# Performance work log

Hardware: AMD Instinct MI355X
Metric: run time of the kernel (lower is better)

Reference implementation:

```python
import jax, jax.numpy as jnp
import numpy as np

B, S, D = 2, 2048, 2048
H, KVH = 16, 4
HD = D // H            # 128
N_REP = H // KVH       # 4


def apply_rope(x, cos, sin):
    # x: (b, s, h, hd); cos/sin: (1, s, 1, hd//2)
    b, s, h, hd = x.shape
    xr = x.reshape(b, s, h, hd // 2, 2)
    p1, p2 = xr[..., 0], xr[..., 1]
    # Original concatenates rotated halves (does NOT re-interleave).
    return jnp.concatenate([p1 * cos - p2 * sin, p2 * cos + p1 * sin], axis=-1)


def setup_inputs() -> dict:
    key = jax.random.key(0)
    ks = jax.random.split(key, 8)
    hidden_states = jax.random.normal(ks[0], (B, S, D), dtype=jnp.float32)
    # additive causal mask (0 on/below diagonal, -1e9 above)
    mask = jnp.where(jnp.tril(jnp.ones((S, S), dtype=bool)), 0.0, -1e9).astype(jnp.float32)
    attention_mask = mask[None, None, :, :]
    cos = jax.random.normal(ks[1], (1, S, 1, HD // 2), dtype=jnp.float32)
    sin = jax.random.normal(ks[2], (1, S, 1, HD // 2), dtype=jnp.float32)
    sc = 1.0 / np.sqrt(D)
    Wq = jax.random.normal(ks[3], (D, H * HD), dtype=jnp.float32) * sc
    Wk = jax.random.normal(ks[4], (D, KVH * HD), dtype=jnp.float32) * sc
    Wv = jax.random.normal(ks[5], (D, KVH * HD), dtype=jnp.float32) * sc
    Wo = jax.random.normal(ks[6], (H * HD, D), dtype=jnp.float32) * sc
    return {"hidden_states": hidden_states, "attention_mask": attention_mask,
            "cos": cos, "sin": sin, "Wq": Wq, "Wk": Wk, "Wv": Wv, "Wo": Wo}


def reference(hidden_states, attention_mask, cos, sin, Wq, Wk, Wv, Wo):
    b, s, _ = hidden_states.shape
    q = (hidden_states @ Wq).reshape(b, s, H, HD)
    k = (hidden_states @ Wk).reshape(b, s, KVH, HD)
    v = (hidden_states @ Wv).reshape(b, s, KVH, HD)
    q = apply_rope(q, cos, sin)
    k = apply_rope(k, cos, sin)
    # GQA: repeat kv heads contiguously (matches expand+reshape)
    k = jnp.repeat(k, N_REP, axis=2)
    v = jnp.repeat(v, N_REP, axis=2)
    # (b, h, s, hd)
    q = q.transpose(0, 2, 1, 3)
    k = k.transpose(0, 2, 1, 3)
    v = v.transpose(0, 2, 1, 3)
    scores = jnp.einsum('bhqd,bhkd->bhqk', q, k) / np.sqrt(HD).astype(np.float32)
    scores = scores + attention_mask
    attn = jax.nn.softmax(scores.astype(jnp.float32), axis=-1)
    out = jnp.einsum('bhqk,bhkd->bhqd', attn, v)
    out = out.transpose(0, 2, 1, 3).reshape(b, s, H * HD)
    return out @ Wo
```

## Files before the change

kernel.cpp:

```cpp
#include <hip/hip_runtime.h>
#include <cstddef>
#include <cstdint>

#define S_LEN 2048
#define DMODEL 2048
#define NH 16
#define NKV 4
#define HD 128
#define BATCH 2
#define MROWS (BATCH * S_LEN)
#define KVD (NKV * HD)
#define QKVSTR 3072
#define NQT (S_LEN / 64)

typedef __attribute__((ext_vector_type(8))) short bf16x8;
typedef __attribute__((ext_vector_type(4))) float floatx4;
typedef __attribute__((ext_vector_type(8))) _Float16 half8;
typedef __attribute__((ext_vector_type(4))) _Float16 half4;
typedef __attribute__((ext_vector_type(2))) _Float16 half2v;

#define QSCALE 0.1275310255f

__device__ inline short f2bf(float f) {
  union { float f; unsigned u; } v; v.f = f;
  unsigned r = v.u + 0x7FFFu + ((v.u >> 16) & 1u);
  return (short)(r >> 16);
}

__device__ inline half2v pack2h(float lo, float hi) {
  union { decltype(__builtin_amdgcn_cvt_pkrtz(0.f, 0.f)) raw; half2v h; } u;
  u.raw = __builtin_amdgcn_cvt_pkrtz(lo, hi);
  return u.h;
}

__device__ __forceinline__ void glds16(const void* g, void* l) {
  __builtin_amdgcn_global_load_lds(
      reinterpret_cast<const int __attribute__((address_space(1)))*>(
          reinterpret_cast<uintptr_t>(g)),
      reinterpret_cast<int __attribute__((address_space(3)))*>(
          reinterpret_cast<uintptr_t>(l)),
      16, 0, 0);
}

__global__ __launch_bounds__(256) void cast_bf16(
    const float* __restrict__ x, short* __restrict__ y)
{
  const size_t i = ((size_t)blockIdx.x * 256 + threadIdx.x) * 8;
  const float4 a = *(const float4*)(x + i);
  const float4 b = *(const float4*)(x + i + 4);
  bf16x8 o;
  o[0] = f2bf(a.x); o[1] = f2bf(a.y); o[2] = f2bf(a.z); o[3] = f2bf(a.w);
  o[4] = f2bf(b.x); o[5] = f2bf(b.y); o[6] = f2bf(b.z); o[7] = f2bf(b.w);
  *(bf16x8*)(y + i) = o;
}

__global__ __launch_bounds__(256) void tcast(
    const float* __restrict__ W, short* __restrict__ Wt, int N)
{
  __shared__ float Ts[64][65];
  const int n0 = blockIdx.x * 64, k0 = blockIdx.y * 64;
  const int tid = threadIdx.x;
#pragma unroll
  for (int it = 0; it < 4; ++it) {
    const int r = it * 16 + (tid >> 4);
    *(float4*)&Ts[r][(tid & 15) * 4] =
        *(const float4*)&W[(size_t)(k0 + r) * N + n0 + (tid & 15) * 4];
  }
  __syncthreads();
  const int n = tid >> 2, kg = (tid & 3) * 16;
  bf16x8 o0, o1;
#pragma unroll
  for (int e = 0; e < 8; ++e) o0[e] = f2bf(Ts[kg + e][n]);
#pragma unroll
  for (int e = 0; e < 8; ++e) o1[e] = f2bf(Ts[kg + 8 + e][n]);
  short* dst = Wt + (size_t)(n0 + n) * DMODEL + k0 + kg;
  *(bf16x8*)dst = o0;
  *(bf16x8*)(dst + 8) = o1;
}

template <bool OUTF16>
__global__ __launch_bounds__(256) void gemm_glds(
    const short* __restrict__ A, const short* __restrict__ Bt,
    void* __restrict__ Cv, int M, int N, int K)
{
  __shared__ short As[128 * 64];
  __shared__ short Bs[128 * 64];

  const int tid = threadIdx.x;
  const int wave = tid >> 6, lane = tid & 63;
  const int l16 = lane & 15, quad = lane >> 4;
  const int wm = (wave & 1) * 64, wn = (wave >> 1) * 64;
  const int m0 = blockIdx.y * 128, n0 = blockIdx.x * 128;

  const short* Ab = A + (size_t)(m0 + wave * 32 + (lane >> 3)) * K + ((lane & 7) << 3);
  const short* Bb = Bt + (size_t)(n0 + wave * 32 + (lane >> 3)) * K + ((lane & 7) << 3);
  short* Asw = As + wave * 32 * 64;
  short* Bsw = Bs + wave * 32 * 64;

  floatx4 acc[4][4];
#pragma unroll
  for (int i = 0; i < 4; ++i)
#pragma unroll
    for (int j = 0; j < 4; ++j)
#pragma unroll
      for (int r = 0; r < 4; ++r) acc[i][j][r] = 0.f;

  for (int k0 = 0; k0 < K; k0 += 64) {
    __syncthreads();
#pragma unroll
    for (int u = 0; u < 4; ++u) {
      glds16(Ab + (size_t)(u * 8) * K + k0, Asw + u * 8 * 64);
      glds16(Bb + (size_t)(u * 8) * K + k0, Bsw + u * 8 * 64);
    }
    __syncthreads();
#pragma unroll
    for (int c = 0; c < 2; ++c) {
      bf16x8 af[4], bf[4];
#pragma unroll
      for (int i = 0; i < 4; ++i)
        af[i] = *(const bf16x8*)&As[(wm + i * 16 + l16) * 64 + c * 32 + quad * 8];
#pragma unroll
      for (int j = 0; j < 4; ++j)
        bf[j] = *(const bf16x8*)&Bs[(wn + j * 16 + l16) * 64 + c * 32 + quad * 8];
#pragma unroll
      for (int i = 0; i < 4; ++i)
#pragma unroll
        for (int j = 0; j < 4; ++j)
          acc[i][j] = __builtin_amdgcn_mfma_f32_16x16x32_bf16(af[i], bf[j], acc[i][j], 0, 0, 0);
    }
  }

#pragma unroll
  for (int i = 0; i < 4; ++i)
#pragma unroll
    for (int r = 0; r < 4; ++r) {
      const int row = m0 + wm + i * 16 + (quad << 2) + r;
      if (OUTF16) {
        _Float16* cr = (_Float16*)Cv + (size_t)row * N + n0 + wn + l16;
#pragma unroll
        for (int j = 0; j < 4; ++j) cr[j * 16] = (_Float16)acc[i][j][r];
      } else {
        float* cr = (float*)Cv + (size_t)row * N + n0 + wn + l16;
#pragma unroll
        for (int j = 0; j < 4; ++j) cr[j * 16] = acc[i][j][r];
      }
    }
}

__global__ __launch_bounds__(256) void rope_k(
    _Float16* __restrict__ kh, const float* __restrict__ cosp,
    const float* __restrict__ sinp)
{
  const int row = blockIdx.x * 4 + (threadIdx.x >> 6);
  const int sl = row & (S_LEN - 1);
  const int t = threadIdx.x & 63;
  const int h = t >> 4, g = t & 15;
  _Float16* base = kh + (size_t)row * QKVSTR + h * HD;
  const half8 x = *(const half8*)(base + 8 * g);
  const float4 c4 = *(const float4*)&cosp[sl * 64 + 4 * g];
  const float4 s4 = *(const float4*)&sinp[sl * 64 + 4 * g];
  const float p1[4] = {(float)x[0], (float)x[2], (float)x[4], (float)x[6]};
  const float p2[4] = {(float)x[1], (float)x[3], (float)x[5], (float)x[7]};
  const float cc[4] = {c4.x, c4.y, c4.z, c4.w};
  const float ss[4] = {s4.x, s4.y, s4.z, s4.w};
  __syncthreads();
  half4 o1, o2;
#pragma unroll
  for (int u = 0; u < 4; ++u) {
    o1[u] = (_Float16)(p1[u] * cc[u] - p2[u] * ss[u]);
    o2[u] = (_Float16)(p2[u] * cc[u] + p1[u] * ss[u]);
  }
  *(half4*)(base + 4 * g) = o1;
  *(half4*)(base + 64 + 4 * g) = o2;
}

__global__ __launch_bounds__(256) void vtprep(
    const _Float16* __restrict__ v, _Float16* __restrict__ Vt)
{
  __shared__ _Float16 Ts[64][72];
  const int s0 = blockIdx.x * 64, c0 = blockIdx.y * 64;
  const int tid = threadIdx.x;
#pragma unroll
  for (int it = 0; it < 4; ++it) {
    const int r = it * 16 + (tid >> 4);
    *(half4*)&Ts[r][(tid & 15) * 4] =
        *(const half4*)&v[(size_t)(s0 + r) * QKVSTR + c0 + (tid & 15) * 4];
  }
  __syncthreads();
  const int dr = tid >> 2, sg = tid & 3;
  const int d = c0 + dr;
  const int kvh = d >> 7, dd = d & 127;
  const int bb = s0 >> 11, sl = s0 & (S_LEN - 1);
  half8 t0, t1;
#pragma unroll
  for (int kk = 0; kk < 8; ++kk) t0[kk] = Ts[sg * 16 + kk][dr];
#pragma unroll
  for (int kk = 0; kk < 8; ++kk) t1[kk] = Ts[sg * 16 + 8 + kk][dr];
  _Float16* dst = Vt + ((size_t)(bb * NKV + kvh) * HD + dd) * S_LEN + sl + sg * 16;
  *(half8*)dst = t0;
  *(half8*)(dst + 8) = t1;
}

__global__ __launch_bounds__(256, 3) void attn_mfma(
    const _Float16* __restrict__ Qh, const _Float16* __restrict__ Kr,
    const _Float16* __restrict__ Vt, const float* __restrict__ cosp,
    const float* __restrict__ sinp, short* __restrict__ aout)
{
  __shared__ _Float16 Ks[64][136];
  __shared__ _Float16 Vs[128][72];
  __shared__ _Float16 Ps[4][16][72];

  const int tid = threadIdx.x;
  const int wave = tid >> 6, lane = tid & 63;
  const int l16 = lane & 15, quad = lane >> 4;
  const int pair = blockIdx.x;
  const int h = blockIdx.y, b = blockIdx.z;
  const int kvh = h >> 2;

  const int skr = tid >> 2;
  const int skc = (tid & 3) * 32;
  const _Float16* kgp = Kr + (size_t)(b * S_LEN + skr) * QKVSTR + kvh * HD + skc;
  const int svr = tid >> 1;
  const int svc = (tid & 1) * 32;
  const _Float16* vgp = Vt + ((size_t)(b * NKV + kvh) * HD + svr) * S_LEN + svc;

  for (int pass = 0; pass < 2; ++pass) {
    const int qt = pass ? (NQT - 1 - pair) : pair;
    const int q0 = qt * 64 + wave * 16;
    const int srow = q0 + l16;

    half8 qf[4];
    {
      const _Float16* qraw = Qh + (size_t)(b * S_LEN + srow) * QKVSTR + h * HD;
#pragma unroll
      for (int cc = 0; cc < 2; ++cc) {
        const half8 r0 = *(const half8*)(qraw + cc * 64 + quad * 16);
        const half8 r1 = *(const half8*)(qraw + cc * 64 + quad * 16 + 8);
        const float4 c0 = *(const float4*)&cosp[srow % S_LEN * 64 + cc * 32 + quad * 8];
        const float4 c1 = *(const float4*)&cosp[srow % S_LEN * 64 + cc * 32 + quad * 8 + 4];
        const float4 s0 = *(const float4*)&sinp[srow % S_LEN * 64 + cc * 32 + quad * 8];
        const float4 s1 = *(const float4*)&sinp[srow % S_LEN * 64 + cc * 32 + quad * 8 + 4];
        const float cA[8] = {c0.x, c0.y, c0.z, c0.w, c1.x, c1.y, c1.z, c1.w};
        const float sA[8] = {s0.x, s0.y, s0.z, s0.w, s1.x, s1.y, s1.z, s1.w};
#pragma unroll
        for (int j = 0; j < 8; ++j) {
          const float p1 = (float)((j < 4) ? r0[2 * j] : r1[2 * (j - 4)]);
          const float p2 = (float)((j < 4) ? r0[2 * j + 1] : r1[2 * (j - 4) + 1]);
          qf[cc][j]     = (_Float16)((p1 * cA[j] - p2 * sA[j]) * QSCALE);
          qf[cc + 2][j] = (_Float16)((p2 * cA[j] + p1 * sA[j]) * QSCALE);
        }
      }
    }

    floatx4 o[8];
#pragma unroll
    for (int d = 0; d < 8; ++d) o[d] = (floatx4){0.f, 0.f, 0.f, 0.f};
    float m_run[4] = {-3e38f, -3e38f, -3e38f, -3e38f};
    float l_run[4] = {0.f, 0.f, 0.f, 0.f};

    for (int kt = 0; kt <= qt; ++kt) {
      const int k0 = kt * 64;
      __syncthreads();
      {
        const _Float16* g = kgp + (size_t)k0 * QKVSTR;
        _Float16* dst = &Ks[skr][skc];
#pragma unroll
        for (int u = 0; u < 4; ++u)
          *(half8*)(dst + u * 8) = *(const half8*)(g + u * 8);
      }
      {
        const _Float16* g = vgp + k0;
        _Float16* dst = &Vs[svr][svc];
#pragma unroll
        for (int u = 0; u < 4; ++u)
          *(half8*)(dst + u * 8) = *(const half8*)(g + u * 8);
      }
      __syncthreads();

      floatx4 s[4];
#pragma unroll
      for (int i = 0; i < 4; ++i) {
        s[i] = (floatx4){0.f, 0.f, 0.f, 0.f};
#pragma unroll
        for (int c = 0; c < 4; ++c) {
          const half8 kf = *(const half8*)&Ks[i * 16 + l16][quad * 8 + c * 32];
          s[i] = __builtin_amdgcn_mfma_f32_16x16x32_f16(qf[c], kf, s[i], 0, 0, 0);
        }
      }

      if (kt == qt) {
#pragma unroll
        for (int i = 0; i < 4; ++i) {
          const int kpos = k0 + i * 16 + l16;
#pragma unroll
          for (int r = 0; r < 4; ++r)
            if (kpos > q0 + quad * 4 + r) s[i][r] = -3.0e38f;
        }
      }

      float p[4][4];
#pragma unroll
      for (int r = 0; r < 4; ++r) {
        float rm = fmaxf(fmaxf(s[0][r], s[1][r]), fmaxf(s[2][r], s[3][r]));
        rm = fmaxf(rm, __shfl_xor(rm, 1));
        rm = fmaxf(rm, __shfl_xor(rm, 2));
        rm = fmaxf(rm, __shfl_xor(rm, 4));
        rm = fmaxf(rm, __shfl_xor(rm, 8));
        const float mnew = fmaxf(m_run[r], rm);
        const float alpha = exp2f(m_run[r] - mnew);
        m_run[r] = mnew;
        float rs = 0.f;
#pragma unroll
        for (int i = 0; i < 4; ++i) { p[i][r] = exp2f(s[i][r] - mnew); rs += p[i][r]; }
        rs += __shfl_xor(rs, 1);
        rs += __shfl_xor(rs, 2);
        rs += __shfl_xor(rs, 4);
        rs += __shfl_xor(rs, 8);
        l_run[r] = l_run[r] * alpha + rs;
#pragma unroll
        for (int d = 0; d < 8; ++d) o[d][r] *= alpha;
      }

      const int odd = l16 & 1;
      const int cbase = l16 & 14;
#pragma unroll
      for (int i = 0; i < 4; ++i) {
#pragma unroll
        for (int rr = 0; rr < 2; ++rr) {
          const float send = odd ? p[i][rr] : p[i][2 + rr];
          const float recv = __shfl_xor(send, 1);
          const float lo = odd ? recv : p[i][rr];
          const float hi = odd ? p[i][2 + rr] : recv;
          *(half2v*)&Ps[wave][quad * 4 + 2 * odd + rr][i * 16 + cbase] = pack2h(lo, hi);
        }
      }
      const half8 pf0 = *(const half8*)&Ps[wave][l16][quad * 8];
      const half8 pf1 = *(const half8*)&Ps[wave][l16][32 + quad * 8];

#pragma unroll
      for (int d = 0; d < 8; ++d) {
        const half8 vf0 = *(const half8*)&Vs[d * 16 + l16][quad * 8];
        const half8 vf1 = *(const half8*)&Vs[d * 16 + l16][32 + quad * 8];
        o[d] = __builtin_amdgcn_mfma_f32_16x16x32_f16(pf0, vf0, o[d], 0, 0, 0);
        o[d] = __builtin_amdgcn_mfma_f32_16x16x32_f16(pf1, vf1, o[d], 0, 0, 0);
      }
    }

    float inv[4];
#pragma unroll
    for (int r = 0; r < 4; ++r) inv[r] = 1.0f / l_run[r];
#pragma unroll
    for (int d = 0; d < 8; ++d)
#pragma unroll
      for (int r = 0; r < 4; ++r)
        aout[(size_t)(b * S_LEN + q0 + quad * 4 + r) * DMODEL + h * HD + d * 16 + l16] =
            f2bf(o[d][r] * inv[r]);
  }
}

extern "C" void kernel_launch(void* const* d_in, const int* in_sizes, int n_in,
                              void* d_out, int out_size, void* d_ws, size_t ws_size,
                              hipStream_t stream) {
  const float* hs   = (const float*)d_in[0];
  const float* cosp = (const float*)d_in[2];
  const float* sinp = (const float*)d_in[3];
  const float* Wq   = (const float*)d_in[4];
  const float* Wk   = (const float*)d_in[5];
  const float* Wv   = (const float*)d_in[6];
  const float* Wo   = (const float*)d_in[7];
  float* out = (float*)d_out;

  char* w = (char*)d_ws;
  short*    hsb = (short*)w;
  short*    Wt  = (short*)(w + 16777216);
  _Float16* qkv = (_Float16*)(w + 29360128);
  _Float16* Vt  = (_Float16*)(w + 54525952);
  short*    ao  = hsb;

  _Float16* qh = qkv;
  _Float16* kh = qkv + 2048;
  _Float16* vh = qkv + 2560;

  dim3 blk(256);
  cast_bf16<<<MROWS * DMODEL / (8 * 256), blk, 0, stream>>>(hs, hsb);
  tcast<<<dim3(DMODEL / 64, DMODEL / 64), blk, 0, stream>>>(Wq, Wt, DMODEL);
  tcast<<<dim3(KVD / 64, DMODEL / 64), blk, 0, stream>>>(Wk, Wt + (size_t)2048 * DMODEL, KVD);
  tcast<<<dim3(KVD / 64, DMODEL / 64), blk, 0, stream>>>(Wv, Wt + (size_t)2560 * DMODEL, KVD);
  gemm_glds<true><<<dim3(QKVSTR / 128, MROWS / 128), blk, 0, stream>>>(hsb, Wt, qkv, MROWS, QKVSTR, DMODEL);
  rope_k<<<MROWS / 4, blk, 0, stream>>>(kh, cosp, sinp);
  vtprep<<<dim3(MROWS / 64, KVD / 64), blk, 0, stream>>>(vh, Vt);
  attn_mfma<<<dim3(NQT / 2, NH, BATCH), blk, 0, stream>>>(qh, kh, Vt, cosp, sinp, ao);
  tcast<<<dim3(DMODEL / 64, DMODEL / 64), blk, 0, stream>>>(Wo, Wt, DMODEL);
  gemm_glds<false><<<dim3(DMODEL / 128, MROWS / 128), blk, 0, stream>>>(ao, Wt, out, MROWS, DMODEL, DMODEL);
}
```

Baseline: 395.6 us.

## Double-buffer K/V tiles with register prefetch in attention kernel

The attention kernel now keeps two LDS buffers for K and V. It issues the global loads for the next tile into registers before computing on the current tile, then stores them into the alternate buffer afterwards, so global latency can overlap MFMA work and one barrier per iteration is removed. MFMA sections are wrapped with s_setprio, and the online-softmax rescale runs only when the row max grows. The extra LDS lowers the occupancy hint from 3 to 2 blocks per CU, and holding the prefetched tile in registers raises register pressure.

```diff
diff --git a/kernel.cpp b/kernel.cpp
--- a/kernel.cpp
+++ b/kernel.cpp
@@ -201,13 +201,13 @@
   *(half8*)(dst + 8) = t1;
 }
 
-__global__ __launch_bounds__(256, 3) void attn_mfma(
+__global__ __launch_bounds__(256, 2) void attn_mfma(
     const _Float16* __restrict__ Qh, const _Float16* __restrict__ Kr,
     const _Float16* __restrict__ Vt, const float* __restrict__ cosp,
     const float* __restrict__ sinp, short* __restrict__ aout)
 {
-  __shared__ _Float16 Ks[64][136];
-  __shared__ _Float16 Vs[128][72];
+  __shared__ _Float16 Ks[2][64][136];
+  __shared__ _Float16 Vs[2][128][72];
   __shared__ _Float16 Ps[4][16][72];
 
   const int tid = threadIdx.x;
@@ -258,35 +258,49 @@
     float m_run[4] = {-3e38f, -3e38f, -3e38f, -3e38f};
     float l_run[4] = {0.f, 0.f, 0.f, 0.f};
 
+    __syncthreads();
+    {
+      _Float16* dst = &Ks[0][skr][skc];
+#pragma unroll
+      for (int u = 0; u < 4; ++u)
+        *(half8*)(dst + u * 8) = *(const half8*)(kgp + u * 8);
+      _Float16* dv = &Vs[0][svr][svc];
+#pragma unroll
+      for (int u = 0; u < 4; ++u)
+        *(half8*)(dv + u * 8) = *(const half8*)(vgp + u * 8);
+    }
+    __syncthreads();
+
+    int cur = 0;
     for (int kt = 0; kt <= qt; ++kt) {
       const int k0 = kt * 64;
-      __syncthreads();
-      {
-        const _Float16* g = kgp + (size_t)k0 * QKVSTR;
-        _Float16* dst = &Ks[skr][skc];
-#pragma unroll
-        for (int u = 0; u < 4; ++u)
-          *(half8*)(dst + u * 8) = *(const half8*)(g + u * 8);
-      }
-      {
-        const _Float16* g = vgp + k0;
-        _Float16* dst = &Vs[svr][svc];
-#pragma unroll
-        for (int u = 0; u < 4; ++u)
-          *(half8*)(dst + u * 8) = *(const half8*)(g + u * 8);
-      }
-      __syncthreads();
+      const bool pre = (kt < qt);
+
+      half8 kreg[4], vreg[4];
+      if (pre) {
+        const _Float16* g = kgp + (size_t)(kt + 1) * 64 * QKVSTR;
+#pragma unroll
+        for (int u = 0; u < 4; ++u) kreg[u] = *(const half8*)(g + u * 8);
+        const _Float16* gv = vgp + (kt + 1) * 64;
+#pragma unroll
+        for (int u = 0; u < 4; ++u) vreg[u] = *(const half8*)(gv + u * 8);
+      }
+
+      const _Float16 (*Kc)[136] = Ks[cur];
+      const _Float16 (*Vc)[72]  = Vs[cur];
 
       floatx4 s[4];
+      __builtin_amdgcn_s_setprio(1);
 #pragma unroll
       for (int i = 0; i < 4; ++i) {
         s[i] = (floatx4){0.f, 0.f, 0.f, 0.f};
 #pragma unroll
         for (int c = 0; c < 4; ++c) {
-          const half8 kf = *(const half8*)&Ks[i * 16 + l16][quad * 8 + c * 32];
+          const half8 kf = *(const half8*)&Kc[i * 16 + l16][quad * 8 + c * 32];
           s[i] = __builtin_amdgcn_mfma_f32_16x16x32_f16(qf[c], kf, s[i], 0, 0, 0);
         }
       }
+      __builtin_amdgcn_s_setprio(0);
 
       if (kt == qt) {
 #pragma unroll
@@ -306,19 +320,21 @@
         rm = fmaxf(rm, __shfl_xor(rm, 2));
         rm = fmaxf(rm, __shfl_xor(rm, 4));
         rm = fmaxf(rm, __shfl_xor(rm, 8));
-        const float mnew = fmaxf(m_run[r], rm);
-        const float alpha = exp2f(m_run[r] - mnew);
-        m_run[r] = mnew;
+        if (rm > m_run[r]) {
+          const float alpha = exp2f(m_run[r] - rm);
+          m_run[r] = rm;
+          l_run[r] *= alpha;
+#pragma unroll
+          for (int d = 0; d < 8; ++d) o[d][r] *= alpha;
+        }
         float rs = 0.f;
 #pragma unroll
-        for (int i = 0; i < 4; ++i) { p[i][r] = exp2f(s[i][r] - mnew); rs += p[i][r]; }
+        for (int i = 0; i < 4; ++i) { p[i][r] = exp2f(s[i][r] - m_run[r]); rs += p[i][r]; }
         rs += __shfl_xor(rs, 1);
         rs += __shfl_xor(rs, 2);
         rs += __shfl_xor(rs, 4);
         rs += __shfl_xor(rs, 8);
-        l_run[r] = l_run[r] * alpha + rs;
-#pragma unroll
-        for (int d = 0; d < 8; ++d) o[d][r] *= alpha;
+        l_run[r] += rs;
       }
 
       const int odd = l16 & 1;
@@ -337,13 +353,26 @@
       const half8 pf0 = *(const half8*)&Ps[wave][l16][quad * 8];
       const half8 pf1 = *(const half8*)&Ps[wave][l16][32 + quad * 8];
 
+      __builtin_amdgcn_s_setprio(1);
 #pragma unroll
       for (int d = 0; d < 8; ++d) {
-        const half8 vf0 = *(const half8*)&Vs[d * 16 + l16][quad * 8];
-        const half8 vf1 = *(const half8*)&Vs[d * 16 + l16][32 + quad * 8];
+        const half8 vf0 = *(const half8*)&Vc[d * 16 + l16][quad * 8];
+        const half8 vf1 = *(const half8*)&Vc[d * 16 + l16][32 + quad * 8];
         o[d] = __builtin_amdgcn_mfma_f32_16x16x32_f16(pf0, vf0, o[d], 0, 0, 0);
         o[d] = __builtin_amdgcn_mfma_f32_16x16x32_f16(pf1, vf1, o[d], 0, 0, 0);
       }
+      __builtin_amdgcn_s_setprio(0);
+
+      if (pre) {
+        _Float16* dst = &Ks[cur ^ 1][skr][skc];
+#pragma unroll
+        for (int u = 0; u < 4; ++u) *(half8*)(dst + u * 8) = kreg[u];
+        _Float16* dv = &Vs[cur ^ 1][svr][svc];
+#pragma unroll
+        for (int u = 0; u < 4; ++u) *(half8*)(dv + u * 8) = vreg[u];
+      }
+      __syncthreads();
+      cur ^= 1;
     }
 
     float inv[4];
```

Measured after the change: 396.1 us. Within noise of the previous version (+0.1%).

## Launch one attention block per query tile, heaviest first, with MFMA priority hints

Applied to the files above, without the earlier changes.

Replaces the paired light/heavy query-tile scheme with one block per query tile. Heads are mapped to the fastest grid dimension, and blocks are ordered from the longest causal range to the shortest, which doubles the block count and lets the scheduler balance load dynamically. It also raises wave priority around the MFMA sections with s_setprio and skips the rescale of the output accumulator when the running max does not grow. The cost is that each block now loads Q and applies rope once per tile, and the new branch inside the softmax can cause divergence.

```diff
diff --git a/kernel.cpp b/kernel.cpp
--- a/kernel.cpp
+++ b/kernel.cpp
@@ -213,8 +213,8 @@
   const int tid = threadIdx.x;
   const int wave = tid >> 6, lane = tid & 63;
   const int l16 = lane & 15, quad = lane >> 4;
-  const int pair = blockIdx.x;
-  const int h = blockIdx.y, b = blockIdx.z;
+  const int h = blockIdx.x, b = blockIdx.z;
+  const int qt = (NQT - 1) - blockIdx.y;
   const int kvh = h >> 2;
 
   const int skr = tid >> 2;
@@ -224,138 +224,142 @@
   const int svc = (tid & 1) * 32;
   const _Float16* vgp = Vt + ((size_t)(b * NKV + kvh) * HD + svr) * S_LEN + svc;
 
-  for (int pass = 0; pass < 2; ++pass) {
-    const int qt = pass ? (NQT - 1 - pair) : pair;
-    const int q0 = qt * 64 + wave * 16;
-    const int srow = q0 + l16;
-
-    half8 qf[4];
+  const int q0 = qt * 64 + wave * 16;
+  const int srow = q0 + l16;
+
+  half8 qf[4];
+  {
+    const _Float16* qraw = Qh + (size_t)(b * S_LEN + srow) * QKVSTR + h * HD;
+    const int co = (srow & (S_LEN - 1)) * 64;
+#pragma unroll
+    for (int cc = 0; cc < 2; ++cc) {
+      const half8 r0 = *(const half8*)(qraw + cc * 64 + quad * 16);
+      const half8 r1 = *(const half8*)(qraw + cc * 64 + quad * 16 + 8);
+      const float4 c0 = *(const float4*)&cosp[co + cc * 32 + quad * 8];
+      const float4 c1 = *(const float4*)&cosp[co + cc * 32 + quad * 8 + 4];
+      const float4 s0 = *(const float4*)&sinp[co + cc * 32 + quad * 8];
+      const float4 s1 = *(const float4*)&sinp[co + cc * 32 + quad * 8 + 4];
+      const float cA[8] = {c0.x, c0.y, c0.z, c0.w, c1.x, c1.y, c1.z, c1.w};
+      const float sA[8] = {s0.x, s0.y, s0.z, s0.w, s1.x, s1.y, s1.z, s1.w};
+#pragma unroll
+      for (int j = 0; j < 8; ++j) {
+        const float p1 = (float)((j < 4) ? r0[2 * j] : r1[2 * (j - 4)]);
+        const float p2 = (float)((j < 4) ? r0[2 * j + 1] : r1[2 * (j - 4) + 1]);
+        qf[cc][j]     = (_Float16)((p1 * cA[j] - p2 * sA[j]) * QSCALE);
+        qf[cc + 2][j] = (_Float16)((p2 * cA[j] + p1 * sA[j]) * QSCALE);
+      }
+    }
+  }
+
+  floatx4 o[8];
+#pragma unroll
+  for (int d = 0; d < 8; ++d) o[d] = (floatx4){0.f, 0.f, 0.f, 0.f};
+  float m_run[4] = {-3e38f, -3e38f, -3e38f, -3e38f};
+  float l_run[4] = {0.f, 0.f, 0.f, 0.f};
+
+  for (int kt = 0; kt <= qt; ++kt) {
+    const int k0 = kt * 64;
+    __syncthreads();
     {
-      const _Float16* qraw = Qh + (size_t)(b * S_LEN + srow) * QKVSTR + h * HD;
-#pragma unroll
-      for (int cc = 0; cc < 2; ++cc) {
-        const half8 r0 = *(const half8*)(qraw + cc * 64 + quad * 16);
-        const half8 r1 = *(const half8*)(qraw + cc * 64 + quad * 16 + 8);
-        const float4 c0 = *(const float4*)&cosp[srow % S_LEN * 64 + cc * 32 + quad * 8];
-        const float4 c1 = *(const float4*)&cosp[srow % S_LEN * 64 + cc * 32 + quad * 8 + 4];
-        const float4 s0 = *(const float4*)&sinp[srow % S_LEN * 64 + cc * 32 + quad * 8];
-        const float4 s1 = *(const float4*)&sinp[srow % S_LEN * 64 + cc * 32 + quad * 8 + 4];
-        const float cA[8] = {c0.x, c0.y, c0.z, c0.w, c1.x, c1.y, c1.z, c1.w};
-        const float sA[8] = {s0.x, s0.y, s0.z, s0.w, s1.x, s1.y, s1.z, s1.w};
-#pragma unroll
-        for (int j = 0; j < 8; ++j) {
-          const float p1 = (float)((j < 4) ? r0[2 * j] : r1[2 * (j - 4)]);
-          const float p2 = (float)((j < 4) ? r0[2 * j + 1] : r1[2 * (j - 4) + 1]);
-          qf[cc][j]     = (_Float16)((p1 * cA[j] - p2 * sA[j]) * QSCALE);
-          qf[cc + 2][j] = (_Float16)((p2 * cA[j] + p1 * sA[j]) * QSCALE);
-        }
-      }
-    }
-
-    floatx4 o[8];
-#pragma unroll
-    for (int d = 0; d < 8; ++d) o[d] = (floatx4){0.f, 0.f, 0.f, 0.f};
-    float m_run[4] = {-3e38f, -3e38f, -3e38f, -3e38f};
-    float l_run[4] = {0.f, 0.f, 0.f, 0.f};
-
-    for (int kt = 0; kt <= qt; ++kt) {
-      const int k0 = kt * 64;
-      __syncthreads();
-      {
-        const _Float16* g = kgp + (size_t)k0 * QKVSTR;
-        _Float16* dst = &Ks[skr][skc];
-#pragma unroll
-        for (int u = 0; u < 4; ++u)
-          *(half8*)(dst + u * 8) = *(const half8*)(g + u * 8);
-      }
-      {
-        const _Float16* g = vgp + k0;
-        _Float16* dst = &Vs[svr][svc];
-#pragma unroll
-        for (int u = 0; u < 4; ++u)
-          *(half8*)(dst + u * 8) = *(const half8*)(g + u * 8);
-      }
-      __syncthreads();
-
-      floatx4 s[4];
+      const _Float16* g = kgp + (size_t)k0 * QKVSTR;
+      _Float16* dst = &Ks[skr][skc];
+#pragma unroll
+      for (int u = 0; u < 4; ++u)
+        *(half8*)(dst + u * 8) = *(const half8*)(g + u * 8);
+    }
+    {
+      const _Float16* g = vgp + k0;
+      _Float16* dst = &Vs[svr][svc];
+#pragma unroll
+      for (int u = 0; u < 4; ++u)
+        *(half8*)(dst + u * 8) = *(const half8*)(g + u * 8);
+    }
+    __syncthreads();
+
+    floatx4 s[4];
+    __builtin_amdgcn_s_setprio(1);
+#pragma unroll
+    for (int i = 0; i < 4; ++i) {
+      s[i] = (floatx4){0.f, 0.f, 0.f, 0.f};
+#pragma unroll
+      for (int c = 0; c < 4; ++c) {
+        const half8 kf = *(const half8*)&Ks[i * 16 + l16][quad * 8 + c * 32];
+        s[i] = __builtin_amdgcn_mfma_f32_16x16x32_f16(qf[c], kf, s[i], 0, 0, 0);
+      }
+    }
+    __builtin_amdgcn_s_setprio(0);
+
+    if (kt == qt) {
 #pragma unroll
       for (int i = 0; i < 4; ++i) {
-        s[i] = (floatx4){0.f, 0.f, 0.f, 0.f};
-#pragma unroll
-        for (int c = 0; c < 4; ++c) {
-          const half8 kf = *(const half8*)&Ks[i * 16 + l16][quad * 8 + c * 32];
-          s[i] = __builtin_amdgcn_mfma_f32_16x16x32_f16(qf[c], kf, s[i], 0, 0, 0);
-        }
-      }
-
-      if (kt == qt) {
-#pragma unroll
-        for (int i = 0; i < 4; ++i) {
-          const int kpos = k0 + i * 16 + l16;
-#pragma unroll
-          for (int r = 0; r < 4; ++r)
-            if (kpos > q0 + quad * 4 + r) s[i][r] = -3.0e38f;
-        }
-      }
-
-      float p[4][4];
-#pragma unroll
-      for (int r = 0; r < 4; ++r) {
-        float rm = fmaxf(fmaxf(s[0][r], s[1][r]), fmaxf(s[2][r], s[3][r]));
-        rm = fmaxf(rm, __shfl_xor(rm, 1));
-        rm = fmaxf(rm, __shfl_xor(rm, 2));
-        rm = fmaxf(rm, __shfl_xor(rm, 4));
-        rm = fmaxf(rm, __shfl_xor(rm, 8));
-        const float mnew = fmaxf(m_run[r], rm);
-        const float alpha = exp2f(m_run[r] - mnew);
-        m_run[r] = mnew;
-        float rs = 0.f;
-#pragma unroll
-        for (int i = 0; i < 4; ++i) { p[i][r] = exp2f(s[i][r] - mnew); rs += p[i][r]; }
-        rs += __shfl_xor(rs, 1);
-        rs += __shfl_xor(rs, 2);
-        rs += __shfl_xor(rs, 4);
-        rs += __shfl_xor(rs, 8);
-        l_run[r] = l_run[r] * alpha + rs;
+        const int kpos = k0 + i * 16 + l16;
+#pragma unroll
+        for (int r = 0; r < 4; ++r)
+          if (kpos > q0 + quad * 4 + r) s[i][r] = -3.0e38f;
+      }
+    }
+
+    float p[4][4];
+#pragma unroll
+    for (int r = 0; r < 4; ++r) {
+      float rm = fmaxf(fmaxf(s[0][r], s[1][r]), fmaxf(s[2][r], s[3][r]));
+      rm = fmaxf(rm, __shfl_xor(rm, 1));
+      rm = fmaxf(rm, __shfl_xor(rm, 2));
+      rm = fmaxf(rm, __shfl_xor(rm, 4));
+      rm = fmaxf(rm, __shfl_xor(rm, 8));
+      if (rm > m_run[r]) {
+        const float alpha = exp2f(m_run[r] - rm);
+        m_run[r] = rm;
+        l_run[r] *= alpha;
 #pragma unroll
         for (int d = 0; d < 8; ++d) o[d][r] *= alpha;
       }
-
-      const int odd = l16 & 1;
-      const int cbase = l16 & 14;
-#pragma unroll
-      for (int i = 0; i < 4; ++i) {
-#pragma unroll
-        for (int rr = 0; rr < 2; ++rr) {
-          const float send = odd ? p[i][rr] : p[i][2 + rr];
-          const float recv = __shfl_xor(send, 1);
-          const float lo = odd ? recv : p[i][rr];
-          const float hi = odd ? p[i][2 + rr] : recv;
-          *(half2v*)&Ps[wave][quad * 4 + 2 * odd + rr][i * 16 + cbase] = pack2h(lo, hi);
-        }
-      }
-      const half8 pf0 = *(const half8*)&Ps[wave][l16][quad * 8];
-      const half8 pf1 = *(const half8*)&Ps[wave][l16][32 + quad * 8];
-
-#pragma unroll
-      for (int d = 0; d < 8; ++d) {
-        const half8 vf0 = *(const half8*)&Vs[d * 16 + l16][quad * 8];
-        const half8 vf1 = *(const half8*)&Vs[d * 16 + l16][32 + quad * 8];
-        o[d] = __builtin_amdgcn_mfma_f32_16x16x32_f16(pf0, vf0, o[d], 0, 0, 0);
-        o[d] = __builtin_amdgcn_mfma_f32_16x16x32_f16(pf1, vf1, o[d], 0, 0, 0);
-      }
-    }
-
-    float inv[4];
-#pragma unroll
-    for (int r = 0; r < 4; ++r) inv[r] = 1.0f / l_run[r];
-#pragma unroll
-    for (int d = 0; d < 8; ++d)
-#pragma unroll
-      for (int r = 0; r < 4; ++r)
-        aout[(size_t)(b * S_LEN + q0 + quad * 4 + r) * DMODEL + h * HD + d * 16 + l16] =
-            f2bf(o[d][r] * inv[r]);
-  }
+      float rs = 0.f;
+#pragma unroll
+      for (int i = 0; i < 4; ++i) { p[i][r] = exp2f(s[i][r] - m_run[r]); rs += p[i][r]; }
+      rs += __shfl_xor(rs, 1);
+      rs += __shfl_xor(rs, 2);
+      rs += __shfl_xor(rs, 4);
+      rs += __shfl_xor(rs, 8);
+      l_run[r] += rs;
+    }
+
+    const int odd = l16 & 1;
+    const int cbase = l16 & 14;
+#pragma unroll
+    for (int i = 0; i < 4; ++i) {
+#pragma unroll
+      for (int rr = 0; rr < 2; ++rr) {
+        const float send = odd ? p[i][rr] : p[i][2 + rr];
+        const float recv = __shfl_xor(send, 1);
+        const float lo = odd ? recv : p[i][rr];
+        const float hi = odd ? p[i][2 + rr] : recv;
+        *(half2v*)&Ps[wave][quad * 4 + 2 * odd + rr][i * 16 + cbase] = pack2h(lo, hi);
+      }
+    }
+    const half8 pf0 = *(const half8*)&Ps[wave][l16][quad * 8];
+    const half8 pf1 = *(const half8*)&Ps[wave][l16][32 + quad * 8];
+
+    __builtin_amdgcn_s_setprio(1);
+#pragma unroll
+    for (int d = 0; d < 8; ++d) {
+      const half8 vf0 = *(const half8*)&Vs[d * 16 + l16][quad * 8];
+      const half8 vf1 = *(const half8*)&Vs[d * 16 + l16][32 + quad * 8];
+      o[d] = __builtin_amdgcn_mfma_f32_16x16x32_f16(pf0, vf0, o[d], 0, 0, 0);
+      o[d] = __builtin_amdgcn_mfma_f32_16x16x32_f16(pf1, vf1, o[d], 0, 0, 0);
+    }
+    __builtin_amdgcn_s_setprio(0);
+  }
+
+  float inv[4];
+#pragma unroll
+  for (int r = 0; r < 4; ++r) inv[r] = 1.0f / l_run[r];
+#pragma unroll
+  for (int d = 0; d < 8; ++d)
+#pragma unroll
+    for (int r = 0; r < 4; ++r)
+      aout[(size_t)(b * S_LEN + q0 + quad * 4 + r) * DMODEL + h * HD + d * 16 + l16] =
+          f2bf(o[d][r] * inv[r]);
 }
 
 extern "C" void kernel_launch(void* const* d_in, const int* in_sizes, int n_in,
@@ -389,7 +393,7 @@
   gemm_glds<true><<<dim3(QKVSTR / 128, MROWS / 128), blk, 0, stream>>>(hsb, Wt, qkv, MROWS, QKVSTR, DMODEL);
   rope_k<<<MROWS / 4, blk, 0, stream>>>(kh, cosp, sinp);
   vtprep<<<dim3(MROWS / 64, KVD / 64), blk, 0, stream>>>(vh, Vt);
-  attn_mfma<<<dim3(NQT / 2, NH, BATCH), blk, 0, stream>>>(qh, kh, Vt, cosp, sinp, ao);
+  attn_mfma<<<dim3(NH, NQT, BATCH), blk, 0, stream>>>(qh, kh, Vt, cosp, sinp, ao);
   tcast<<<dim3(DMODEL / 64, DMODEL / 64), blk, 0, stream>>>(Wo, Wt, DMODEL);
   gemm_glds<false><<<dim3(DMODEL / 128, MROWS / 128), blk, 0, stream>>>(ao, Wt, out, MROWS, DMODEL, DMODEL);
 }
```

Result: no change. 399.0 us (+0.9%).
